# Optimization experiments

Measured on AMD Instinct MI355X. Metric: run time of the kernel, lower is better.

Reference implementation:

```python
import jax, jax.numpy as jnp
import numpy as np

D_IN = 1024
D_OUT = 1024
NUM_HEADS = 16
HEAD_DIM = D_OUT // NUM_HEADS


def setup_inputs() -> dict:
    key = jax.random.key(0)
    k1, k2, k3, k4 = jax.random.split(key, 4)
    x = jax.random.normal(k1, (2, 2048, D_IN), dtype=jnp.float32)
    # qkv Linear (bias=False): weight [3*d_out, d_in]
    w_qkv = jax.random.normal(k2, (3 * D_OUT, D_IN), dtype=jnp.float32) * (1.0 / np.sqrt(D_IN))
    # proj Linear (default bias=True): weight [d_out, d_out], bias [d_out]
    w_proj = jax.random.normal(k3, (D_OUT, D_OUT), dtype=jnp.float32) * (1.0 / np.sqrt(D_OUT))
    b_proj = jax.random.normal(k4, (D_OUT,), dtype=jnp.float32) * 0.01
    return {"x": x, "w_qkv": w_qkv, "w_proj": w_proj, "b_proj": b_proj}


def reference(x, w_qkv, w_proj, b_proj):
    B, S, E = x.shape
    qkv = jnp.einsum("bse,fe->bsf", x, w_qkv)                 # [B,S,3*d_out]
    qkv = qkv.reshape(B, S, 3, NUM_HEADS, HEAD_DIM)
    qkv = jnp.transpose(qkv, (2, 0, 3, 1, 4))                  # [3,B,H,S,D]
    q, k, v = qkv[0], qkv[1], qkv[2]
    scores = jnp.einsum("bhqd,bhkd->bhqk", q, k)               # [B,H,S,S]
    causal = jnp.triu(jnp.ones((S, S), dtype=bool), k=1)
    scores = jnp.where(causal, -jnp.inf, scores)
    # NOTE: source divides by head_dim**(-0.5), i.e. multiplies by sqrt(head_dim)
    scores = scores / (HEAD_DIM ** -0.5)
    attn = jax.nn.softmax(scores, axis=-1)
    ctx = jnp.einsum("bhqk,bhkd->bhqd", attn, v)               # [B,H,S,D]
    ctx = jnp.transpose(ctx, (0, 2, 1, 3)).reshape(B, S, E)
    return jnp.einsum("bse,fe->bsf", ctx, w_proj) + b_proj
```

## Files before the change

### kernel.cpp

```cpp
#include <hip/hip_runtime.h>

typedef _Float16 f16;
typedef _Float16 f16x4 __attribute__((ext_vector_type(4)));
typedef _Float16 f16x8 __attribute__((ext_vector_type(8)));
typedef float f32x4 __attribute__((ext_vector_type(4)));

#define MFMA16(a, b, c) __builtin_amdgcn_mfma_f32_16x16x32_f16(a, b, c, 0, 0, 0)
#define QSCALE 11.5415603f

typedef const __attribute__((address_space(1))) void* gp1_t;
typedef __attribute__((address_space(3))) void* lp3_t;
__device__ __forceinline__ void gld16(const void* g, void* l) {
    __builtin_amdgcn_global_load_lds((gp1_t)g, (lp3_t)l, 16, 0, 0);
}

__global__ __launch_bounds__(256) void cvt_all(
    const float* __restrict__ x, const float* __restrict__ wq, const float* __restrict__ wp,
    f16* __restrict__ xh, f16* __restrict__ wqh, f16* __restrict__ wph)
{
    int i = blockIdx.x * 256 + threadIdx.x;
    const float4* src; f16x4* dst; int off;
    if (i < 1048576)      { src = (const float4*)x;  dst = (f16x4*)xh;  off = i; }
    else if (i < 1835008) { src = (const float4*)wq; dst = (f16x4*)wqh; off = i - 1048576; }
    else                  { src = (const float4*)wp; dst = (f16x4*)wph; off = i - 1835008; }
    float4 v = src[off];
    f16x4 o = { (f16)v.x, (f16)v.y, (f16)v.z, (f16)v.w };
    dst[off] = o;
}

template<int EPI>
__global__ __launch_bounds__(256) void gemm_k(
    const f16* __restrict__ A, const f16* __restrict__ B, int K,
    f16* __restrict__ qb, f16* __restrict__ kb, f16* __restrict__ vt,
    float* __restrict__ outF, const float* __restrict__ bias)
{
    __shared__ f16 as[128 * 32];
    __shared__ f16 bs[128 * 32];
    const int t = threadIdx.x;
    const int m0 = blockIdx.y * 128, n0 = blockIdx.x * 128;
    const int lane = t & 63, wv = t >> 6;
    const int wm = wv >> 1, wn = wv & 1;
    const int lr = lane & 15, g = lane >> 4;
    const int srow = lane >> 2, schk = (lane & 3) * 8;
    const f16* Ab = A + (size_t)m0 * K;
    const f16* Bb = B + (size_t)n0 * K;
    f32x4 acc[4][4] = {};

    for (int k0 = 0; k0 < K; k0 += 32) {
        __syncthreads();
        #pragma unroll
        for (int i2 = 0; i2 < 2; ++i2) {
            const int r0 = wv * 32 + i2 * 16;
            gld16(&Ab[(size_t)(r0 + srow) * K + k0 + schk], &as[r0 * 32]);
            gld16(&Bb[(size_t)(r0 + srow) * K + k0 + schk], &bs[r0 * 32]);
        }
        __syncthreads();
        f16x8 af[4], bf[4];
        #pragma unroll
        for (int mt = 0; mt < 4; ++mt)
            af[mt] = *reinterpret_cast<const f16x8*>(&as[(wm * 64 + mt * 16 + lr) * 32 + g * 8]);
        #pragma unroll
        for (int nt = 0; nt < 4; ++nt)
            bf[nt] = *reinterpret_cast<const f16x8*>(&bs[(wn * 64 + nt * 16 + lr) * 32 + g * 8]);
        #pragma unroll
        for (int mt = 0; mt < 4; ++mt)
            #pragma unroll
            for (int nt = 0; nt < 4; ++nt)
                acc[mt][nt] = MFMA16(af[mt], bf[nt], acc[mt][nt]);
    }

    #pragma unroll
    for (int mt = 0; mt < 4; ++mt) {
        #pragma unroll
        for (int nt = 0; nt < 4; ++nt) {
            const int n = n0 + wn * 64 + nt * 16 + lr;
            const int s0 = m0 + wm * 64 + mt * 16 + 4 * g;
            if (EPI == 0) {
                const int which = n >> 10, h = (n >> 6) & 15, d = n & 63;
                const int b = s0 >> 11, s = s0 & 2047;
                if (which == 2) {
                    f16x4 vv;
                    #pragma unroll
                    for (int i = 0; i < 4; ++i) vv[i] = (f16)acc[mt][nt][i];
                    *reinterpret_cast<f16x4*>(&vt[((size_t)((b << 4) + h) * 64 + d) * 2048 + s]) = vv;
                } else {
                    f16* dst = which ? kb : qb;
                    const float sc = which ? 1.0f : QSCALE;
                    #pragma unroll
                    for (int i = 0; i < 4; ++i)
                        dst[((size_t)((b << 4) + h) * 2048 + (s + i)) * 64 + d] = (f16)(acc[mt][nt][i] * sc);
                }
            } else {
                #pragma unroll
                for (int i = 0; i < 4; ++i)
                    outF[(size_t)(s0 + i) * 1024 + n] = acc[mt][nt][i] + bias[n];
            }
        }
    }
}

__global__ __launch_bounds__(64) void attn_k(
    const f16* __restrict__ Q, const f16* __restrict__ K, const f16* __restrict__ VT,
    f16* __restrict__ ctx, f16* __restrict__ opart,
    float* __restrict__ mpart, float* __restrict__ lpart)
{
    __shared__ f16 lp[32][72];
    const int lane = threadIdx.x;
    const int lr = lane & 15, g = lane >> 4;
    const int bid = blockIdx.x;
    int j, s; bool split;
    if (bid < 2048) { split = true;  j = 63 - (bid >> 6); s = (bid >> 5) & 1; }
    else            { split = false; j = 31 - ((bid - 2048) >> 5); s = 0; }
    const int bh = bid & 31;
    const int b = bh >> 4, h = bh & 15;
    const size_t base = (size_t)bh * (2048 * 64);
    const f16* Qb = Q + base;
    const f16* Kb = K + base;
    const f16* Vb = VT + base;
    const int q0 = j << 5;
    const int ntt = (j >> 1) + 1;
    const int H = (ntt + 1) >> 1;
    const int t0 = split ? (s ? H : 0) : 0;
    const int t1 = split ? (s ? ntt : H) : ntt;
    const bool diag = (t1 == ntt);

    f16x8 qf[2][2];
    #pragma unroll
    for (int nt = 0; nt < 2; ++nt)
        #pragma unroll
        for (int ks = 0; ks < 2; ++ks)
            qf[nt][ks] = *reinterpret_cast<const f16x8*>(&Qb[(size_t)(q0 + nt * 16 + lr) * 64 + ks * 32 + g * 8]);

    f32x4 o[4][2] = {};
    float mrun[2] = { -1e30f, -1e30f };
    float lsum[2] = { 0.f, 0.f };

#define ATTN_TILE(KV0, MTMAX, MASKED) do {                                              \
    const int kv0_ = (KV0);                                                             \
    f32x4 st[MTMAX][2] = {};                                                            \
    _Pragma("unroll")                                                                   \
    for (int mt = 0; mt < MTMAX; ++mt) {                                                \
        f16x8 ak[2];                                                                    \
        _Pragma("unroll")                                                               \
        for (int ks = 0; ks < 2; ++ks)                                                  \
            ak[ks] = *reinterpret_cast<const f16x8*>(                                   \
                &Kb[(size_t)(kv0_ + mt * 16 + lr) * 64 + ks * 32 + g * 8]);             \
        _Pragma("unroll")                                                               \
        for (int nt = 0; nt < 2; ++nt)                                                  \
            _Pragma("unroll")                                                           \
            for (int ks = 0; ks < 2; ++ks)                                              \
                st[mt][nt] = MFMA16(ak[ks], qf[nt][ks], st[mt][nt]);                    \
    }                                                                                   \
    _Pragma("unroll")                                                                   \
    for (int nt = 0; nt < 2; ++nt) {                                                    \
        const int qrow_ = q0 + nt * 16 + lr;                                            \
        float mloc = -1e30f;                                                            \
        _Pragma("unroll")                                                               \
        for (int mt = 0; mt < MTMAX; ++mt)                                              \
            _Pragma("unroll")                                                           \
            for (int i = 0; i < 4; ++i) {                                               \
                float sv = st[mt][nt][i];                                               \
                if (MASKED) {                                                           \
                    int kkk = kv0_ + mt * 16 + 4 * g + i;                               \
                    sv = (kkk <= qrow_) ? sv : -1e30f;                                  \
                    st[mt][nt][i] = sv;                                                 \
                }                                                                       \
                mloc = fmaxf(mloc, sv);                                                 \
            }                                                                           \
        mloc = fmaxf(mloc, __shfl_xor(mloc, 16));                                       \
        mloc = fmaxf(mloc, __shfl_xor(mloc, 32));                                       \
        if (__any(mloc > mrun[nt] + 8.0f)) {                             \
            float mnew = fmaxf(mrun[nt], mloc);                                         \
            float sc = exp2f(mrun[nt] - mnew);                                          \
            lsum[nt] *= sc;                                                             \
            _Pragma("unroll")                                                           \
            for (int mo = 0; mo < 4; ++mo)                                              \
                _Pragma("unroll")                                                       \
                for (int i = 0; i < 4; ++i) o[mo][nt][i] *= sc;                         \
            mrun[nt] = mnew;                                                            \
        }                                                                               \
        float ls = 0.f;                                                                 \
        _Pragma("unroll")                                                               \
        for (int mt = 0; mt < MTMAX; ++mt) {                                            \
            f16x4 pk;                                                                   \
            _Pragma("unroll")                                                           \
            for (int i = 0; i < 4; ++i) {                                               \
                float p = exp2f(st[mt][nt][i] - mrun[nt]);                              \
                ls += p; pk[i] = (f16)p;                                                \
            }                                                                           \
            *reinterpret_cast<f16x4*>(&lp[nt * 16 + lr][mt * 16 + 4 * g]) = pk;         \
        }                                                                               \
        lsum[nt] += ls;                                                                 \
    }                                                                                   \
    {                                                                                   \
        constexpr int PVKS = (MTMAX) / 2;                                               \
        f16x8 pf[2][PVKS];                                                              \
        _Pragma("unroll")                                                               \
        for (int nt = 0; nt < 2; ++nt)                                                  \
            _Pragma("unroll")                                                           \
            for (int ks = 0; ks < PVKS; ++ks)                                           \
                pf[nt][ks] = *reinterpret_cast<const f16x8*>(                           \
                    &lp[nt * 16 + lr][ks * 32 + g * 8]);                                \
        _Pragma("unroll")                                                               \
        for (int mo = 0; mo < 4; ++mo) {                                                \
            f16x8 av[PVKS];                                                             \
            _Pragma("unroll")                                                           \
            for (int ks = 0; ks < PVKS; ++ks)                                           \
                av[ks] = *reinterpret_cast<const f16x8*>(                               \
                    &Vb[(size_t)(mo * 16 + lr) * 2048 + kv0_ + ks * 32 + g * 8]);       \
            _Pragma("unroll")                                                           \
            for (int nt = 0; nt < 2; ++nt)                                              \
                _Pragma("unroll")                                                       \
                for (int ks = 0; ks < PVKS; ++ks)                                       \
                    o[mo][nt] = MFMA16(av[ks], pf[nt][ks], o[mo][nt]);                  \
        }                                                                               \
    }                                                                                   \
} while (0)

    const int tEnd = t1 - (diag ? 1 : 0);
    for (int tt = t0; tt < tEnd; ++tt)
        ATTN_TILE(tt << 6, 4, false);
    if (diag) {
        const int kvl = (ntt - 1) << 6;
        if (j & 1) ATTN_TILE(kvl, 4, true);
        else       ATTN_TILE(kvl, 2, true);
    }
#undef ATTN_TILE

    #pragma unroll
    for (int nt = 0; nt < 2; ++nt) {
        float l = lsum[nt];
        l += __shfl_xor(l, 16);
        l += __shfl_xor(l, 32);
        const float inv = 1.0f / l;
        const int ql = nt * 16 + lr;
        if (!split) {
            const size_t rowoff = ((size_t)(b * 2048 + q0 + ql)) * 1024 + h * 64;
            #pragma unroll
            for (int mo = 0; mo < 4; ++mo) {
                f16x4 ov;
                #pragma unroll
                for (int i = 0; i < 4; ++i) ov[i] = (f16)(o[mo][nt][i] * inv);
                *reinterpret_cast<f16x4*>(&ctx[rowoff + mo * 16 + 4 * g]) = ov;
            }
        } else {
            const int mi = ((s * 32 + bh) * 32 + (j - 32)) * 32 + ql;
            #pragma unroll
            for (int mo = 0; mo < 4; ++mo) {
                f16x4 ov;
                #pragma unroll
                for (int i = 0; i < 4; ++i) ov[i] = (f16)(o[mo][nt][i] * inv);
                *reinterpret_cast<f16x4*>(&opart[(size_t)mi * 64 + mo * 16 + 4 * g]) = ov;
            }
            if (g == 0) { mpart[mi] = mrun[nt]; lpart[mi] = l; }
        }
    }
}

__global__ __launch_bounds__(256) void combine_k(
    const f16* __restrict__ opart, const float* __restrict__ mpart,
    const float* __restrict__ lpart, f16* __restrict__ ctx)
{
    const int blk = blockIdx.x;
    const int bh = blk >> 5, jj = blk & 31;
    const int b = bh >> 4, h = bh & 15;
    const int t = threadIdx.x;
    const int q = t >> 3, dc = (t & 7) * 8;
    const int mi0 = (bh * 32 + jj) * 32 + q;
    const int mi1 = mi0 + 32768;
    const float m0 = mpart[mi0], m1 = mpart[mi1];
    const float l0 = lpart[mi0], l1 = lpart[mi1];
    const float mx = fmaxf(m0, m1);
    const float a0 = l0 * exp2f(m0 - mx);
    const float a1 = l1 * exp2f(m1 - mx);
    const float r = 1.0f / (a0 + a1);
    const float c0 = a0 * r, c1 = a1 * r;
    f16x8 v0 = *reinterpret_cast<const f16x8*>(&opart[(size_t)mi0 * 64 + dc]);
    f16x8 v1 = *reinterpret_cast<const f16x8*>(&opart[(size_t)mi1 * 64 + dc]);
    f16x8 outv;
    #pragma unroll
    for (int i = 0; i < 8; ++i) outv[i] = (f16)(c0 * (float)v0[i] + c1 * (float)v1[i]);
    const int qg = (jj + 32) * 32 + q;
    *reinterpret_cast<f16x8*>(&ctx[((size_t)(b * 2048 + qg)) * 1024 + h * 64 + dc]) = outv;
}

extern "C" void kernel_launch(void* const* d_in, const int* in_sizes, int n_in,
                              void* d_out, int out_size, void* d_ws, size_t ws_size,
                              hipStream_t stream) {
    const float* x      = (const float*)d_in[0];
    const float* w_qkv  = (const float*)d_in[1];
    const float* w_proj = (const float*)d_in[2];
    const float* b_proj = (const float*)d_in[3];
    float* out = (float*)d_out;

    char* p = (char*)d_ws;
    f16* xh     = (f16*)p; p += (size_t)4096 * 1024 * 2;
    f16* wqkvh  = (f16*)p; p += (size_t)3072 * 1024 * 2;
    f16* wprojh = (f16*)p; p += (size_t)1024 * 1024 * 2;
    f16* qbuf   = (f16*)p; p += (size_t)2 * 16 * 2048 * 64 * 2;
    f16* kbuf   = (f16*)p; p += (size_t)2 * 16 * 2048 * 64 * 2;
    f16* vtbuf  = (f16*)p; p += (size_t)2 * 16 * 64 * 2048 * 2;
    f16* ctx    = (f16*)p; p += (size_t)4096 * 1024 * 2;

    f16*   opart = xh;
    float* mpart = (float*)wqkvh;
    float* lpart = mpart + 65536;

    cvt_all<<<8192, 256, 0, stream>>>(x, w_qkv, w_proj, xh, wqkvh, wprojh);

    gemm_k<0><<<dim3(24, 32), 256, 0, stream>>>(xh, wqkvh, 1024, qbuf, kbuf, vtbuf, nullptr, nullptr);

    attn_k<<<3072, 64, 0, stream>>>(qbuf, kbuf, vtbuf, ctx, opart, mpart, lpart);

    combine_k<<<1024, 256, 0, stream>>>(opart, mpart, lpart, ctx);

    gemm_k<1><<<dim3(8, 32), 256, 0, stream>>>(ctx, wprojh, 1024, nullptr, nullptr, nullptr, out, b_proj);
}
```

Before: 223.5 us.

## Split attention query tiles into up to three KV chunks by causal length

Replaces the fixed two-way split (second half of queries only) with a variable split: query tiles are divided into 1, 2 or 3 KV chunks depending on their causal length. Every tile now writes partial results, and the combine kernel merges up to three partials for all rows. The goal is to balance per-workgroup work across the causal triangle and raise parallelism. In exchange it launches more blocks, some of which return immediately, and it adds partial-buffer traffic plus a combine step for every row.

```diff
diff --git a/kernel.cpp b/kernel.cpp
--- a/kernel.cpp
+++ b/kernel.cpp
@@ -13,6 +13,9 @@
 __device__ __forceinline__ void gld16(const void* g, void* l) {
     __builtin_amdgcn_global_load_lds((gp1_t)g, (lp3_t)l, 16, 0, 0);
 }
+
+__device__ __forceinline__ int unit_nc(int j)     { return j < 22 ? 1 : (j < 44 ? 2 : 3); }
+__device__ __forceinline__ int unit_prefix(int j) { return j < 22 ? j : (j < 44 ? 22 + 2 * (j - 22) : 66 + 3 * (j - 44)); }
 
 __global__ __launch_bounds__(256) void cvt_all(
     const float* __restrict__ x, const float* __restrict__ wq, const float* __restrict__ wp,
@@ -101,28 +104,29 @@
 
 __global__ __launch_bounds__(64) void attn_k(
     const f16* __restrict__ Q, const f16* __restrict__ K, const f16* __restrict__ VT,
-    f16* __restrict__ ctx, f16* __restrict__ opart,
-    float* __restrict__ mpart, float* __restrict__ lpart)
+    f16* __restrict__ opart, float* __restrict__ mpart, float* __restrict__ lpart)
 {
     __shared__ f16 lp[32][72];
     const int lane = threadIdx.x;
     const int lr = lane & 15, g = lane >> 4;
     const int bid = blockIdx.x;
-    int j, s; bool split;
-    if (bid < 2048) { split = true;  j = 63 - (bid >> 6); s = (bid >> 5) & 1; }
-    else            { split = false; j = 31 - ((bid - 2048) >> 5); s = 0; }
     const int bh = bid & 31;
-    const int b = bh >> 4, h = bh & 15;
+    const int rest = bid >> 5;
+    const int j = 63 - rest / 3;
+    const int c = rest % 3;
+    const int ntt = (j >> 1) + 1;
+    const int nc = unit_nc(j);
+    if (c >= nc) return;
+    const int cbase = ntt / nc, crem = ntt - cbase * nc;
+    const int start = c * cbase + (c < crem ? c : crem);
+    const int len = cbase + (c < crem ? 1 : 0);
+    const bool diag = (start + len == ntt);
+
     const size_t base = (size_t)bh * (2048 * 64);
     const f16* Qb = Q + base;
     const f16* Kb = K + base;
     const f16* Vb = VT + base;
     const int q0 = j << 5;
-    const int ntt = (j >> 1) + 1;
-    const int H = (ntt + 1) >> 1;
-    const int t0 = split ? (s ? H : 0) : 0;
-    const int t1 = split ? (s ? ntt : H) : ntt;
-    const bool diag = (t1 == ntt);
 
     f16x8 qf[2][2];
     #pragma unroll
@@ -217,8 +221,8 @@
     }                                                                                   \
 } while (0)
 
-    const int tEnd = t1 - (diag ? 1 : 0);
-    for (int tt = t0; tt < tEnd; ++tt)
+    const int tEnd = start + len - (diag ? 1 : 0);
+    for (int tt = start; tt < tEnd; ++tt)
         ATTN_TILE(tt << 6, 4, false);
     if (diag) {
         const int kvl = (ntt - 1) << 6;
@@ -227,6 +231,7 @@
     }
 #undef ATTN_TILE
 
+    const int slot = bh * 126 + unit_prefix(j) + c;
     #pragma unroll
     for (int nt = 0; nt < 2; ++nt) {
         float l = lsum[nt];
@@ -234,26 +239,15 @@
         l += __shfl_xor(l, 32);
         const float inv = 1.0f / l;
         const int ql = nt * 16 + lr;
-        if (!split) {
-            const size_t rowoff = ((size_t)(b * 2048 + q0 + ql)) * 1024 + h * 64;
+        const int mi = slot * 32 + ql;
+        #pragma unroll
+        for (int mo = 0; mo < 4; ++mo) {
+            f16x4 ov;
             #pragma unroll
-            for (int mo = 0; mo < 4; ++mo) {
-                f16x4 ov;
-                #pragma unroll
-                for (int i = 0; i < 4; ++i) ov[i] = (f16)(o[mo][nt][i] * inv);
-                *reinterpret_cast<f16x4*>(&ctx[rowoff + mo * 16 + 4 * g]) = ov;
-            }
-        } else {
-            const int mi = ((s * 32 + bh) * 32 + (j - 32)) * 32 + ql;
-            #pragma unroll
-            for (int mo = 0; mo < 4; ++mo) {
-                f16x4 ov;
-                #pragma unroll
-                for (int i = 0; i < 4; ++i) ov[i] = (f16)(o[mo][nt][i] * inv);
-                *reinterpret_cast<f16x4*>(&opart[(size_t)mi * 64 + mo * 16 + 4 * g]) = ov;
-            }
-            if (g == 0) { mpart[mi] = mrun[nt]; lpart[mi] = l; }
+            for (int i = 0; i < 4; ++i) ov[i] = (f16)(o[mo][nt][i] * inv);
+            *reinterpret_cast<f16x4*>(&opart[(size_t)mi * 64 + mo * 16 + 4 * g]) = ov;
         }
+        if (g == 0) { mpart[mi] = mrun[nt]; lpart[mi] = l; }
     }
 }
 
@@ -262,25 +256,35 @@
     const float* __restrict__ lpart, f16* __restrict__ ctx)
 {
     const int blk = blockIdx.x;
-    const int bh = blk >> 5, jj = blk & 31;
+    const int bh = blk & 31, j = blk >> 5;
     const int b = bh >> 4, h = bh & 15;
+    const int nc = unit_nc(j);
+    const int slot0 = bh * 126 + unit_prefix(j);
     const int t = threadIdx.x;
     const int q = t >> 3, dc = (t & 7) * 8;
-    const int mi0 = (bh * 32 + jj) * 32 + q;
-    const int mi1 = mi0 + 32768;
-    const float m0 = mpart[mi0], m1 = mpart[mi1];
-    const float l0 = lpart[mi0], l1 = lpart[mi1];
-    const float mx = fmaxf(m0, m1);
-    const float a0 = l0 * exp2f(m0 - mx);
-    const float a1 = l1 * exp2f(m1 - mx);
-    const float r = 1.0f / (a0 + a1);
-    const float c0 = a0 * r, c1 = a1 * r;
-    f16x8 v0 = *reinterpret_cast<const f16x8*>(&opart[(size_t)mi0 * 64 + dc]);
-    f16x8 v1 = *reinterpret_cast<const f16x8*>(&opart[(size_t)mi1 * 64 + dc]);
+
+    float m[3], l[3];
+    float M = -1e30f;
+    for (int cc = 0; cc < nc; ++cc) {
+        m[cc] = mpart[(slot0 + cc) * 32 + q];
+        l[cc] = lpart[(slot0 + cc) * 32 + q];
+        M = fmaxf(M, m[cc]);
+    }
+    float wsum = 0.f, w[3];
+    for (int cc = 0; cc < nc; ++cc) { w[cc] = l[cc] * exp2f(m[cc] - M); wsum += w[cc]; }
+    const float r = 1.0f / wsum;
+
+    float acc[8] = {};
+    for (int cc = 0; cc < nc; ++cc) {
+        const float coef = w[cc] * r;
+        f16x8 v = *reinterpret_cast<const f16x8*>(&opart[(size_t)((slot0 + cc) * 32 + q) * 64 + dc]);
+        #pragma unroll
+        for (int i = 0; i < 8; ++i) acc[i] += coef * (float)v[i];
+    }
     f16x8 outv;
     #pragma unroll
-    for (int i = 0; i < 8; ++i) outv[i] = (f16)(c0 * (float)v0[i] + c1 * (float)v1[i]);
-    const int qg = (jj + 32) * 32 + q;
+    for (int i = 0; i < 8; ++i) outv[i] = (f16)acc[i];
+    const int qg = j * 32 + q;
     *reinterpret_cast<f16x8*>(&ctx[((size_t)(b * 2048 + qg)) * 1024 + h * 64 + dc]) = outv;
 }
 
@@ -302,17 +306,17 @@
     f16* vtbuf  = (f16*)p; p += (size_t)2 * 16 * 64 * 2048 * 2;
     f16* ctx    = (f16*)p; p += (size_t)4096 * 1024 * 2;
 
-    f16*   opart = xh;
-    float* mpart = (float*)wqkvh;
-    float* lpart = mpart + 65536;
+    f16*   opart = (f16*)d_out;
+    float* mpart = (float*)xh;
+    float* lpart = mpart + 129024;
 
     cvt_all<<<8192, 256, 0, stream>>>(x, w_qkv, w_proj, xh, wqkvh, wprojh);
 
     gemm_k<0><<<dim3(24, 32), 256, 0, stream>>>(xh, wqkvh, 1024, qbuf, kbuf, vtbuf, nullptr, nullptr);
 
-    attn_k<<<3072, 64, 0, stream>>>(qbuf, kbuf, vtbuf, ctx, opart, mpart, lpart);
-
-    combine_k<<<1024, 256, 0, stream>>>(opart, mpart, lpart, ctx);
+    attn_k<<<6144, 64, 0, stream>>>(qbuf, kbuf, vtbuf, opart, mpart, lpart);
+
+    combine_k<<<2048, 256, 0, stream>>>(opart, mpart, lpart, ctx);
 
     gemm_k<1><<<dim3(8, 32), 256, 0, stream>>>(ctx, wprojh, 1024, nullptr, nullptr, nullptr, out, b_proj);
 }
```

Result: no change. 222.2 us (-0.6%).
